# Kernel tuning notes

Hardware: AMD Instinct MI355X
Metric: run time of the kernel (lower is better)

## Reference

```python
import jax, jax.numpy as jnp
import numpy as np

N = 20000      # nodes
E = 320000     # edges (avg degree 16)
IN = 512       # input feature dim
HID = 64       # hidden_dim
NH = 8         # n_heads
NC = 20        # n_classes
NG = 64        # graphs in batch
EPS = 1e-5     # batchnorm eps


def setup_inputs() -> dict:
    key = jax.random.key(0)
    ks = jax.random.split(key, 32)
    rn = lambda k, shape, s=0.05: (jax.random.normal(k, shape, jnp.float32) * s)
    inp = {
        "x": rn(ks[0], (N, IN), 1.0),
        "src": jax.random.randint(ks[1], (E,), 0, N),
        "dst": jax.random.randint(ks[2], (E,), 0, N),
        "graph_ids": jnp.sort(jax.random.randint(ks[3], (N,), 0, NG)),
        "n_graphs": NG,
        # encoder
        "W_enc": rn(ks[4], (IN, HID)), "b_enc": jnp.zeros((HID,), jnp.float32),
        # GAT layer 0
        "fc_W0": rn(ks[5], (HID, NH * HID)),
        "attn_l0": rn(ks[6], (NH, HID)), "attn_r0": rn(ks[7], (NH, HID)),
        "res_W0": rn(ks[8], (HID, NH * HID)),
        "bias0": jnp.zeros((NH * HID,), jnp.float32),
        "dp_W0": rn(ks[9], (NH * HID, HID)), "dp_b0": jnp.zeros((HID,), jnp.float32),
        # GAT layer 1
        "fc_W1": rn(ks[10], (HID, NH * HID)),
        "attn_l1": rn(ks[11], (NH, HID)), "attn_r1": rn(ks[12], (NH, HID)),
        "res_W1": rn(ks[13], (HID, NH * HID)),
        "bias1": jnp.zeros((NH * HID,), jnp.float32),
        "dp_W1": rn(ks[14], (NH * HID, HID)), "dp_b1": jnp.zeros((HID,), jnp.float32),
        # batchnorm affine
        "gamma": jnp.ones((2 * HID,), jnp.float32), "beta": jnp.zeros((2 * HID,), jnp.float32),
        # global attention pooling gate
        "gate_W": rn(ks[15], (2 * HID, 1)), "gate_b": jnp.zeros((1,), jnp.float32),
        # classifier
        "cls_W": rn(ks[16], (2 * HID, NC)), "cls_b": jnp.zeros((NC,), jnp.float32),
    }
    return inp


def gat_conv(h, fc_W, attn_l, attn_r, res_W, bias, src, dst, n_nodes):
    # DGL GATConv: fc -> per-head scalar scores -> edge softmax over incoming
    # edges -> weighted sum -> residual + bias -> leaky_relu activation.
    nh, d = attn_l.shape
    feat = (h @ fc_W).reshape(n_nodes, nh, d)              # [N,H,D]
    el = jnp.sum(feat * attn_l[None], axis=-1)             # [N,H]
    er = jnp.sum(feat * attn_r[None], axis=-1)             # [N,H]
    e = jax.nn.leaky_relu(el[src] + er[dst], 0.2)          # [E,H]
    m = jax.ops.segment_max(e, dst, num_segments=n_nodes)  # segment softmax
    ex = jnp.exp(e - m[dst])
    denom = jax.ops.segment_sum(ex, dst, num_segments=n_nodes)
    a = ex / denom[dst]                                    # [E,H]
    msg = feat[src] * a[:, :, None]                        # [E,H,D]  (dominant)
    rst = jax.ops.segment_sum(msg, dst, num_segments=n_nodes)  # [N,H,D]
    rst = rst + (h @ res_W).reshape(n_nodes, nh, d) + bias.reshape(nh, d)
    return jax.nn.leaky_relu(rst, 0.01)  # F.leaky_relu default slope


def reference(x, W_enc, b_enc,
              fc_W0, attn_l0, attn_r0, res_W0, bias0, dp_W0, dp_b0,
              fc_W1, attn_l1, attn_r1, res_W1, bias1, dp_W1, dp_b1,
              gamma, beta, gate_W, gate_b, cls_W, cls_b,
              src, dst, graph_ids, n_graphs):
    n_nodes = x.shape[0]
    he = x @ W_enc + b_enc                                  # encoder [N,HID]
    h = he
    h = gat_conv(h, fc_W0, attn_l0, attn_r0, res_W0, bias0, src, dst, n_nodes)
    h = h.reshape(n_nodes, -1) @ dp_W0 + dp_b0              # down_proj 0
    h = gat_conv(h, fc_W1, attn_l1, attn_r1, res_W1, bias1, src, dst, n_nodes)
    h = h.reshape(n_nodes, -1) @ dp_W1 + dp_b1              # down_proj 1
    hg = jnp.concatenate([h, he], axis=1)                   # [N,2*HID]
    # BatchNorm1d (training-mode batch stats, biased variance)
    mu = jnp.mean(hg, axis=0)
    var = jnp.var(hg, axis=0)
    hg = (hg - mu) * jax.lax.rsqrt(var + EPS) * gamma + beta
    # GlobalAttentionPooling: per-graph softmax over node gates
    gate = hg @ gate_W + gate_b                             # [N,1]
    gm = jax.ops.segment_max(gate, graph_ids, num_segments=n_graphs)
    ge = jnp.exp(gate - gm[graph_ids])
    gden = jax.ops.segment_sum(ge, graph_ids, num_segments=n_graphs)
    alpha = ge / gden[graph_ids]                            # [N,1]
    readout = jax.ops.segment_sum(alpha * hg, graph_ids, num_segments=n_graphs)
    return readout @ cls_W + cls_b                          # [NG,NC]
```

## Files before the change

### kernel.cpp

```cpp
#include <hip/hip_runtime.h>
#include <hip/hip_bf16.h>

#define MROWS   20000
#define N_EDGES 320000
#define DIN     512
#define HID     64
#define NH      8
#define ND      512
#define NCLS    20
#define NG      64
#define BN_EPS  1e-5f
#define PCH     16
#define BNB     256
#define TPB     128

typedef __hip_bfloat16 bf16;
typedef __attribute__((ext_vector_type(8))) short s16x8;
typedef __attribute__((ext_vector_type(4))) short s16x4;
typedef __attribute__((ext_vector_type(4))) float f32x4;

enum { TF32 = 0, TBF16 = 1, TMODE = 2 };

__device__ __forceinline__ int is_bf16_mode(const void* gamma) {
    return *(const unsigned*)gamma != 0x3F800000u;
}

__device__ __forceinline__ float ld_f32(const void* p, size_t i) { return ((const float*)p)[i]; }
__device__ __forceinline__ float ld_b16(const void* p, size_t i) { return __bfloat162float(((const bf16*)p)[i]); }

template<int T>
__device__ __forceinline__ float ldT(const void* p, size_t i, int bf) {
    if constexpr (T == TF32) return ld_f32(p, i);
    else if constexpr (T == TBF16) return ld_b16(p, i);
    else return bf ? ld_b16(p, i) : ld_f32(p, i);
}
template<int T>
__device__ __forceinline__ void stT(void* p, size_t i, int bf, float v) {
    if constexpr (T == TF32) ((float*)p)[i] = v;
    else if constexpr (T == TBF16) ((bf16*)p)[i] = __float2bfloat16(v);
    else { if (bf) ((bf16*)p)[i] = __float2bfloat16(v); else ((float*)p)[i] = v; }
}

__device__ __forceinline__ float bfbits2f(short s) {
    return __uint_as_float(((unsigned)(unsigned short)s) << 16);
}
__device__ __forceinline__ short f2bfbits(float v) {
    bf16 b = __float2bfloat16(v);
    return *reinterpret_cast<short*>(&b);
}

struct TP { const void* src[7]; bf16* dst[7]; int K[7]; };
__global__ void prep_kernel(TP tp, const void* __restrict__ gamma, int* __restrict__ zero0) {
    int b = blockIdx.x;
    int z = b * 256 + threadIdx.x;
    if (z < 2 * MROWS) zero0[z] = 0;
    const int bf = is_bf16_mode(gamma);
    int id = b / TPB;
    int i = (b - id * TPB) * 256 + threadIdx.x;
    int K = tp.K[id];
    int N = (DIN * HID) / K;
    int n = i / K, k = i - n * K;
    tp.dst[id][i] = __float2bfloat16(ldT<TMODE>(tp.src[id], (size_t)k * N + n, bf));
}

__global__ void hist_kernel(const int* __restrict__ keys, int* __restrict__ counts, int n) {
    int i = blockIdx.x * 256 + threadIdx.x;
    if (i < n) atomicAdd(&counts[keys[i]], 1);
}

__global__ __launch_bounds__(1024)
void scan_all_kernel(const int* __restrict__ counts, int* __restrict__ offs,
                     const int* __restrict__ gids, int* __restrict__ goffs) {
    if (threadIdx.x <= NG) {
        int g = threadIdx.x;
        int lo = 0, hi = MROWS;
        while (lo < hi) {
            int mid = (lo + hi) >> 1;
            if (gids[mid] < g) lo = mid + 1; else hi = mid;
        }
        goffs[g] = lo;
    }
    __shared__ int wsum[16];
    __shared__ int carry_s;
    int carry = 0;
    int lane = threadIdx.x & 63, wid = threadIdx.x >> 6;
    const int NCHUNK = (MROWS + 1023) / 1024;
    for (int ch = 0; ch < NCHUNK; ++ch) {
        int i = ch * 1024 + threadIdx.x;
        int v = (i < MROWS) ? counts[i] : 0;
        int s = v;
        #pragma unroll
        for (int o = 1; o < 64; o <<= 1) { int t = __shfl_up(s, o, 64); if (lane >= o) s += t; }
        if (lane == 63) wsum[wid] = s;
        __syncthreads();
        if (wid == 0 && lane < 16) {
            int t = wsum[lane];
            #pragma unroll
            for (int o = 1; o < 16; o <<= 1) { int u = __shfl_up(t, o, 64); if (lane >= o) t += u; }
            wsum[lane] = t;
        }
        __syncthreads();
        int wc = (wid > 0) ? wsum[wid - 1] : 0;
        int incl = s + wc + carry;
        if (i < MROWS) offs[i] = incl - v;
        if (threadIdx.x == 1023) carry_s = incl;
        __syncthreads();
        carry = carry_s;
    }
    if (threadIdx.x == 0) offs[MROWS] = carry;
}

__global__ void scatter_kernel(const int* __restrict__ src, const int* __restrict__ dst,
                               const int* __restrict__ offs, int* __restrict__ cursor,
                               int* __restrict__ src_sorted) {
    int e = blockIdx.x * 256 + threadIdx.x;
    if (e < N_EDGES) {
        int d = dst[e];
        int pos = offs[d] + atomicAdd(&cursor[d], 1);
        src_sorted[pos] = src[e];
    }
}

template<int K, int NB, int NTOT, bool XF32>
__global__ __launch_bounds__(256)
void gemm_mfma(const void* __restrict__ Araw, const bf16* __restrict__ BT,
               const void* __restrict__ bias, bf16* __restrict__ C,
               const void* __restrict__ gamma) {
    const int bf = is_bf16_mode(gamma);
    const int wid  = threadIdx.x >> 6;
    const int lane = threadIdx.x & 63;
    const int quad = lane >> 4;
    const int l16  = lane & 15;
    const int rb = blockIdx.x * 128 + wid * 32;
    const int cb = blockIdx.y * NB;
    constexpr int CT = NB / 16;
    constexpr int KC = K / 32;

    f32x4 acc[2][CT] = {};
    int r0 = rb + l16;       if (r0 >= MROWS) r0 = MROWS - 1;
    int r1 = rb + 16 + l16;  if (r1 >= MROWS) r1 = MROWS - 1;

    auto lda = [&](int row, int koff) -> s16x8 {
        if (XF32 && !bf) {
            const float* fp = (const float*)Araw + (size_t)row * K + koff;
            float4 u = *(const float4*)fp;
            float4 v = *(const float4*)(fp + 4);
            s16x8 r;
            r[0] = f2bfbits(u.x); r[1] = f2bfbits(u.y); r[2] = f2bfbits(u.z); r[3] = f2bfbits(u.w);
            r[4] = f2bfbits(v.x); r[5] = f2bfbits(v.y); r[6] = f2bfbits(v.z); r[7] = f2bfbits(v.w);
            return r;
        }
        return *(const s16x8*)((const bf16*)Araw + (size_t)row * K + koff);
    };
    const bf16* btp = BT + (size_t)(cb + l16) * K + quad * 8;

    for (int kc = 0; kc < KC; ++kc) {
        s16x8 af0 = lda(r0, quad * 8 + kc * 32);
        s16x8 af1 = lda(r1, quad * 8 + kc * 32);
        s16x8 bfr[CT];
        #pragma unroll
        for (int ct = 0; ct < CT; ++ct)
            bfr[ct] = *(const s16x8*)(btp + (size_t)ct * 16 * K + kc * 32);
        #pragma unroll
        for (int ct = 0; ct < CT; ++ct) {
            acc[0][ct] = __builtin_amdgcn_mfma_f32_16x16x32_bf16(bfr[ct], af0, acc[0][ct], 0, 0, 0);
            acc[1][ct] = __builtin_amdgcn_mfma_f32_16x16x32_bf16(bfr[ct], af1, acc[1][ct], 0, 0, 0);
        }
    }
    #pragma unroll
    for (int ct = 0; ct < CT; ++ct) {
        int c0 = cb + ct * 16 + quad * 4;
        float b0 = bias ? ldT<TMODE>(bias, c0 + 0, bf) : 0.f;
        float b1 = bias ? ldT<TMODE>(bias, c0 + 1, bf) : 0.f;
        float b2 = bias ? ldT<TMODE>(bias, c0 + 2, bf) : 0.f;
        float b3 = bias ? ldT<TMODE>(bias, c0 + 3, bf) : 0.f;
        #pragma unroll
        for (int rt = 0; rt < 2; ++rt) {
            int row = rb + rt * 16 + l16;
            if (row < MROWS) {
                s16x4 o;
                o[0] = f2bfbits(acc[rt][ct][0] + b0);
                o[1] = f2bfbits(acc[rt][ct][1] + b1);
                o[2] = f2bfbits(acc[rt][ct][2] + b2);
                o[3] = f2bfbits(acc[rt][ct][3] + b3);
                *(s16x4*)(C + (size_t)row * NTOT + c0) = o;
            }
        }
    }
}

__global__ __launch_bounds__(256)
void gemm_fcres(const bf16* __restrict__ A, const bf16* __restrict__ BT_fc,
                const bf16* __restrict__ BT_res, const void* __restrict__ bias,
                const void* __restrict__ attn_l, const void* __restrict__ attn_r,
                bf16* __restrict__ feat, bf16* __restrict__ rst,
                float* __restrict__ el, float* __restrict__ er,
                const void* __restrict__ gamma) {
    const int bf = is_bf16_mode(gamma);
    const bool isres = blockIdx.y >= 4;
    const int yy = blockIdx.y & 3;
    const bf16* BT = isres ? BT_res : BT_fc;
    bf16* C = isres ? rst : feat;
    const int wid  = threadIdx.x >> 6;
    const int lane = threadIdx.x & 63;
    const int quad = lane >> 4;
    const int l16  = lane & 15;
    const int rb = blockIdx.x * 128 + wid * 32;
    const int cb = yy * 128;
    constexpr int CT = 8;
    constexpr int K  = HID;
    constexpr int KC = K / 32;

    f32x4 acc[2][CT] = {};
    int r0 = rb + l16;       if (r0 >= MROWS) r0 = MROWS - 1;
    int r1 = rb + 16 + l16;  if (r1 >= MROWS) r1 = MROWS - 1;
    const bf16* a0p = A + (size_t)r0 * K + quad * 8;
    const bf16* a1p = A + (size_t)r1 * K + quad * 8;
    const bf16* btp = BT + (size_t)(cb + l16) * K + quad * 8;

    #pragma unroll
    for (int kc = 0; kc < KC; ++kc) {
        s16x8 af0 = *(const s16x8*)(a0p + kc * 32);
        s16x8 af1 = *(const s16x8*)(a1p + kc * 32);
        s16x8 bfr[CT];
        #pragma unroll
        for (int ct = 0; ct < CT; ++ct)
            bfr[ct] = *(const s16x8*)(btp + (size_t)ct * 16 * K + kc * 32);
        #pragma unroll
        for (int ct = 0; ct < CT; ++ct) {
            acc[0][ct] = __builtin_amdgcn_mfma_f32_16x16x32_bf16(bfr[ct], af0, acc[0][ct], 0, 0, 0);
            acc[1][ct] = __builtin_amdgcn_mfma_f32_16x16x32_bf16(bfr[ct], af1, acc[1][ct], 0, 0, 0);
        }
    }
    #pragma unroll
    for (int ct = 0; ct < CT; ++ct) {
        int c0 = cb + ct * 16 + quad * 4;
        float b0 = isres ? ldT<TMODE>(bias, c0 + 0, bf) : 0.f;
        float b1 = isres ? ldT<TMODE>(bias, c0 + 1, bf) : 0.f;
        float b2 = isres ? ldT<TMODE>(bias, c0 + 2, bf) : 0.f;
        float b3 = isres ? ldT<TMODE>(bias, c0 + 3, bf) : 0.f;
        #pragma unroll
        for (int rt = 0; rt < 2; ++rt) {
            int row = rb + rt * 16 + l16;
            if (row < MROWS) {
                s16x4 o;
                o[0] = f2bfbits(acc[rt][ct][0] + b0);
                o[1] = f2bfbits(acc[rt][ct][1] + b1);
                o[2] = f2bfbits(acc[rt][ct][2] + b2);
                o[3] = f2bfbits(acc[rt][ct][3] + b3);
                *(s16x4*)(C + (size_t)row * ND + c0) = o;
            }
        }
    }
    if (!isres) {
        #pragma unroll
        for (int rt = 0; rt < 2; ++rt) {
            float e0 = 0.f, f0 = 0.f, e1 = 0.f, f1 = 0.f;
            #pragma unroll
            for (int ct = 0; ct < 4; ++ct) {
                int c0 = cb + ct * 16 + quad * 4;
                int c1 = c0 + 64;
                #pragma unroll
                for (int rg = 0; rg < 4; ++rg) {
                    e0 += acc[rt][ct][rg]     * ldT<TMODE>(attn_l, c0 + rg, bf);
                    f0 += acc[rt][ct][rg]     * ldT<TMODE>(attn_r, c0 + rg, bf);
                    e1 += acc[rt][ct + 4][rg] * ldT<TMODE>(attn_l, c1 + rg, bf);
                    f1 += acc[rt][ct + 4][rg] * ldT<TMODE>(attn_r, c1 + rg, bf);
                }
            }
            e0 += __shfl_xor(e0, 16, 64); e0 += __shfl_xor(e0, 32, 64);
            f0 += __shfl_xor(f0, 16, 64); f0 += __shfl_xor(f0, 32, 64);
            e1 += __shfl_xor(e1, 16, 64); e1 += __shfl_xor(e1, 32, 64);
            f1 += __shfl_xor(f1, 16, 64); f1 += __shfl_xor(f1, 32, 64);
            int row = rb + rt * 16 + l16;
            if (row < MROWS) {
                if (quad == 0)      el[row * 8 + 2 * yy]     = e0;
                else if (quad == 1) el[row * 8 + 2 * yy + 1] = e1;
                else if (quad == 2) er[row * 8 + 2 * yy]     = f0;
                else                er[row * 8 + 2 * yy + 1] = f1;
            }
        }
    }
}

__global__ __launch_bounds__(256)
void agg_kernel(const bf16* __restrict__ feat, const float* __restrict__ el,
                const float* __restrict__ er, const int* __restrict__ offs,
                const int* __restrict__ srcs, bf16* __restrict__ rst) {
    int gid = blockIdx.x * 256 + threadIdx.x;
    int n = gid >> 6;
    int l = threadIdx.x & 63;
    if (n >= MROWS) return;
    int hh = l >> 3;
    int e0 = __builtin_amdgcn_readfirstlane(offs[n]);
    int e1 = __builtin_amdgcn_readfirstlane(offs[n + 1]);
    float er_h = er[n * 8 + hh];
    float acc[8] = {0.f, 0.f, 0.f, 0.f, 0.f, 0.f, 0.f, 0.f};
    float den = 0.f;
    for (int base = e0; base < e1; base += 64) {
        int cnt = min(64, e1 - base);
        int sv = (base + l < e1) ? srcs[base + l] : 0;
        for (int eb = 0; eb < cnt; eb += 8) {
            int en = cnt - eb;
            s16x8 ff[8];
            float elv[8];
            int lastv = cnt - 1;
            #pragma unroll
            for (int p = 0; p < 8; ++p) {
                int idx = eb + p; if (idx > lastv) idx = lastv;
                int s = __shfl(sv, idx, 64);
                ff[p] = *(const s16x8*)(feat + (size_t)s * ND + l * 8);
                elv[p] = el[s * 8 + hh];
            }
            float ww[8];
            #pragma unroll
            for (int p = 0; p < 8; ++p) {
                float sc = elv[p] + er_h;
                sc = sc > 0.f ? sc : 0.2f * sc;
                ww[p] = __expf(fminf(sc, 30.f));
            }
            if (en < 8) {
                #pragma unroll
                for (int p = 1; p < 8; ++p)
                    if (p >= en) ww[p] = 0.f;
            }
            #pragma unroll
            for (int p = 0; p < 8; ++p) {
                den += ww[p];
                #pragma unroll
                for (int j = 0; j < 8; ++j)
                    acc[j] += bfbits2f(ff[p][j]) * ww[p];
            }
        }
    }
    float inv = (den > 0.f) ? 1.f / den : 0.f;
    s16x8* rp = (s16x8*)(rst + (size_t)n * ND + l * 8);
    s16x8 rr = *rp;
    s16x8 ro;
    #pragma unroll
    for (int j = 0; j < 8; ++j) {
        float r = bfbits2f(rr[j]) + acc[j] * inv;
        r = r > 0.f ? r : 0.01f * r;
        ro[j] = f2bfbits(r);
    }
    *rp = ro;
}

__global__ void bn_part_kernel(const bf16* __restrict__ h2, const bf16* __restrict__ he,
                               float* __restrict__ psum, float* __restrict__ psq) {
    int t = threadIdx.x;
    int b = blockIdx.x;
    int beg = (int)((long)MROWS * b / BNB);
    int end = (int)((long)MROWS * (b + 1) / BNB);
    const bf16* srcb = (t < 64) ? h2 : he;
    int col = t & 63;
    float s = 0.f, s2 = 0.f;
    for (int r = beg; r < end; ++r) {
        float v = __bfloat162float(srcb[(size_t)r * 64 + col]);
        s += v;
        s2 += v * v;
    }
    psum[b * 128 + t] = s;
    psq[b * 128 + t] = s2;
}

__global__ void bn_reduce_kernel(const float* __restrict__ psum, const float* __restrict__ psq,
                                 const void* __restrict__ gamma, const void* __restrict__ beta,
                                 float* __restrict__ scale, float* __restrict__ shift) {
    const int bf = is_bf16_mode(gamma);
    int t = threadIdx.x;
    float s = 0.f, s2 = 0.f;
    for (int b = 0; b < BNB; ++b) { s += psum[b * 128 + t]; s2 += psq[b * 128 + t]; }
    float mu = s * (1.f / MROWS);
    float var = s2 * (1.f / MROWS) - mu * mu;
    float inv = rsqrtf(fmaxf(var, 0.f) + BN_EPS);
    float a = ldT<TMODE>(gamma, t, bf) * inv;
    scale[t] = a;
    shift[t] = ldT<TMODE>(beta, t, bf) - mu * a;
}

__global__ __launch_bounds__(128)
void poolgate_kernel(const bf16* __restrict__ h2, const bf16* __restrict__ he,
                     const float* __restrict__ scale, const float* __restrict__ shift,
                     const void* __restrict__ gate_W, const void* __restrict__ gate_b,
                     const int* __restrict__ goffs,
                     float* __restrict__ pacc, float* __restrict__ pden,
                     const void* __restrict__ gamma) {
    const int bf = is_bf16_mode(gamma);
    int g = blockIdx.x;
    int c = blockIdx.y;
    int t = threadIdx.x;
    int r0 = goffs[g], r1 = goffs[g + 1];
    int len = r1 - r0;
    int beg = r0 + (int)((long)len * c / PCH);
    int end = r0 + (int)((long)len * (c + 1) / PCH);
    const bf16* srcb = (t < 64) ? h2 : he;
    int col = t & 63;
    float sc = scale[t], sh = shift[t];
    float gw = ldT<TMODE>(gate_W, t, bf);
    float gb = ldT<TMODE>(gate_b, 0, bf);
    __shared__ float ws[2];
    float acc = 0.f, den = 0.f;
    for (int r = beg; r < end; ++r) {
        float v = __bfloat162float(srcb[(size_t)r * 64 + col]) * sc + sh;
        float p = v * gw;
        #pragma unroll
        for (int o = 32; o > 0; o >>= 1) p += __shfl_xor(p, o, 64);
        if ((t & 63) == 0) ws[t >> 6] = p;
        __syncthreads();
        float wg = __expf(fminf(fmaxf(ws[0] + ws[1] + gb, -60.f), 30.f));
        den += wg;
        acc += wg * v;
        __syncthreads();
    }
    pacc[((size_t)g * PCH + c) * 128 + t] = acc;
    if (t == 0) pden[g * PCH + c] = den;
}

__global__ __launch_bounds__(128)
void poolcls_kernel(const float* __restrict__ pacc, const float* __restrict__ pden,
                    const void* __restrict__ W, const void* __restrict__ b,
                    void* __restrict__ out, const void* __restrict__ gamma) {
    const int bf = is_bf16_mode(gamma);
    int g = blockIdx.x;
    int t = threadIdx.x;
    float acc = 0.f, den = 0.f;
    #pragma unroll
    for (int c = 0; c < PCH; ++c) {
        acc += pacc[((size_t)g * PCH + c) * 128 + t];
        den += pden[g * PCH + c];
    }
    __shared__ float rs[128];
    rs[t] = (den > 0.f) ? acc / den : 0.f;
    __syncthreads();
    if (t < NCLS) {
        float o = ldT<TMODE>(b, t, bf);
        #pragma unroll 8
        for (int k = 0; k < 128; ++k)
            o += rs[k] * ldT<TMODE>(W, (size_t)k * NCLS + t, bf);
        stT<TMODE>(out, g * NCLS + t, bf, o);
    }
}

extern "C" void kernel_launch(void* const* d_in, const int* in_sizes, int n_in,
                              void* d_out, int out_size, void* d_ws, size_t ws_size,
                              hipStream_t stream) {
    const void* x       = d_in[0];
    const int*  src     = (const int*)d_in[1];
    const int*  dst     = (const int*)d_in[2];
    const int*  gids    = (const int*)d_in[3];
    const void* W_enc   = d_in[5];
    const void* b_enc   = d_in[6];
    const void* fc_W0   = d_in[7];
    const void* attn_l0 = d_in[8];
    const void* attn_r0 = d_in[9];
    const void* res_W0  = d_in[10];
    const void* bias0   = d_in[11];
    const void* dp_W0   = d_in[12];
    const void* dp_b0   = d_in[13];
    const void* fc_W1   = d_in[14];
    const void* attn_l1 = d_in[15];
    const void* attn_r1 = d_in[16];
    const void* res_W1  = d_in[17];
    const void* bias1   = d_in[18];
    const void* dp_W1   = d_in[19];
    const void* dp_b1   = d_in[20];
    const void* gamma   = d_in[21];
    const void* beta    = d_in[22];
    const void* gate_W  = d_in[23];
    const void* gate_b  = d_in[24];
    const void* cls_W   = d_in[25];
    const void* cls_b   = d_in[26];

    char* wsc = (char*)d_ws;
    size_t off = 0;
    auto alloc = [&](size_t bytes) -> void* {
        void* p = wsc + off;
        off = (off + bytes + 255) & ~(size_t)255;
        return p;
    };
    bf16*  he        = (bf16*) alloc((size_t)MROWS * HID * 2);
    bf16*  h         = (bf16*) alloc((size_t)MROWS * HID * 2);
    bf16*  h2        = (bf16*) alloc((size_t)MROWS * HID * 2);
    bf16*  feat      = (bf16*) alloc((size_t)MROWS * ND * 2);
    bf16*  rst       = (bf16*) alloc((size_t)MROWS * ND * 2);
    bf16*  bt_enc    = (bf16*) alloc((size_t)DIN * HID * 2);
    bf16*  bt_fc0    = (bf16*) alloc((size_t)HID * ND * 2);
    bf16*  bt_res0   = (bf16*) alloc((size_t)HID * ND * 2);
    bf16*  bt_dp0    = (bf16*) alloc((size_t)ND * HID * 2);
    bf16*  bt_fc1    = (bf16*) alloc((size_t)HID * ND * 2);
    bf16*  bt_res1   = (bf16*) alloc((size_t)HID * ND * 2);
    bf16*  bt_dp1    = (bf16*) alloc((size_t)ND * HID * 2);
    float* el        = (float*)alloc((size_t)MROWS * 8 * 4);
    float* er        = (float*)alloc((size_t)MROWS * 8 * 4);
    int*   src_sorted= (int*)  alloc((size_t)N_EDGES * 4);
    int*   offs      = (int*)  alloc((size_t)(MROWS + 1) * 4);
    int*   goffs     = (int*)  alloc((size_t)(NG + 1) * 4);
    float* psum      = (float*)alloc((size_t)BNB * 128 * 4);
    float* psq       = (float*)alloc((size_t)BNB * 128 * 4);
    float* pacc      = (float*)alloc((size_t)NG * PCH * 128 * 4);
    float* pden      = (float*)alloc((size_t)NG * PCH * 4);
    float* bnscale   = (float*)alloc(128 * 4);
    float* bnshift   = (float*)alloc(128 * 4);
    char*  zbase     = (char*) alloc((size_t)MROWS * 4 * 2);
    int* counts  = (int*)zbase;
    int* cursor  = counts + MROWS;

    TP tp;
    tp.src[0] = W_enc;  tp.K[0] = DIN;
    tp.src[1] = fc_W0;  tp.K[1] = HID;
    tp.src[2] = res_W0; tp.K[2] = HID;
    tp.src[3] = dp_W0;  tp.K[3] = ND;
    tp.src[4] = fc_W1;  tp.K[4] = HID;
    tp.src[5] = res_W1; tp.K[5] = HID;
    tp.src[6] = dp_W1;  tp.K[6] = ND;
    tp.dst[0] = bt_enc; tp.dst[1] = bt_fc0; tp.dst[2] = bt_res0; tp.dst[3] = bt_dp0;
    tp.dst[4] = bt_fc1; tp.dst[5] = bt_res1; tp.dst[6] = bt_dp1;
    prep_kernel<<<7 * TPB, 256, 0, stream>>>(tp, gamma, (int*)zbase);

    hist_kernel<<<(N_EDGES + 255) / 256, 256, 0, stream>>>(dst, counts, N_EDGES);
    scan_all_kernel<<<1, 1024, 0, stream>>>(counts, offs, gids, goffs);
    scatter_kernel<<<(N_EDGES + 255) / 256, 256, 0, stream>>>(src, dst, offs, cursor, src_sorted);

    const int GX = (MROWS + 127) / 128;

    gemm_mfma<DIN, 64, 64, true><<<dim3(GX, 1), 256, 0, stream>>>(x, bt_enc, b_enc, he, gamma);

    gemm_fcres<<<dim3(GX, 8), 256, 0, stream>>>(he, bt_fc0, bt_res0, bias0, attn_l0, attn_r0,
                                                feat, rst, el, er, gamma);
    agg_kernel<<<(MROWS * 64) / 256, 256, 0, stream>>>(feat, el, er, offs, src_sorted, rst);
    gemm_mfma<ND, 64, 64, false><<<dim3(GX, 1), 256, 0, stream>>>(rst, bt_dp0, dp_b0, h, gamma);

    gemm_fcres<<<dim3(GX, 8), 256, 0, stream>>>(h, bt_fc1, bt_res1, bias1, attn_l1, attn_r1,
                                                feat, rst, el, er, gamma);
    agg_kernel<<<(MROWS * 64) / 256, 256, 0, stream>>>(feat, el, er, offs, src_sorted, rst);
    gemm_mfma<ND, 64, 64, false><<<dim3(GX, 1), 256, 0, stream>>>(rst, bt_dp1, dp_b1, h2, gamma);

    bn_part_kernel<<<BNB, 128, 0, stream>>>(h2, he, psum, psq);
    bn_reduce_kernel<<<1, 128, 0, stream>>>(psum, psq, gamma, beta, bnscale, bnshift);
    poolgate_kernel<<<dim3(NG, PCH), 128, 0, stream>>>(h2, he, bnscale, bnshift, gate_W, gate_b,
                                                       goffs, pacc, pden, gamma);
    poolcls_kernel<<<NG, 128, 0, stream>>>(pacc, pden, cls_W, cls_b, d_out, gamma);
}
```

Baseline: 470.2 us.

## Split GAT aggregation per head across blocks with 8-lane node groups

The edge-softmax aggregation kernel now gives each block a single head and a chunk of 160 nodes. Each 8-lane group handles one node's 64 head features and walks its incoming edges four at a time. Previously a whole wave processed one node across all heads and shared source indices through shuffles. The new mapping is meant to give more independent node streams per wave and keep each block's gathers within one head's feature slice, which should help L2 locality. In exchange, every lane group reloads source indices and el values itself, and each 16-byte gather covers only one head's slice of a source row.

```diff
diff --git a/kernel.cpp b/kernel.cpp
--- a/kernel.cpp
+++ b/kernel.cpp
@@ -13,6 +13,8 @@
 #define PCH     16
 #define BNB     256
 #define TPB     128
+#define AGG_NBLK  125
+#define AGG_CHUNK 160
 
 typedef __hip_bfloat16 bf16;
 typedef __attribute__((ext_vector_type(8))) short s16x8;
@@ -287,63 +289,62 @@
 void agg_kernel(const bf16* __restrict__ feat, const float* __restrict__ el,
                 const float* __restrict__ er, const int* __restrict__ offs,
                 const int* __restrict__ srcs, bf16* __restrict__ rst) {
-    int gid = blockIdx.x * 256 + threadIdx.x;
-    int n = gid >> 6;
-    int l = threadIdx.x & 63;
-    if (n >= MROWS) return;
-    int hh = l >> 3;
-    int e0 = __builtin_amdgcn_readfirstlane(offs[n]);
-    int e1 = __builtin_amdgcn_readfirstlane(offs[n + 1]);
-    float er_h = er[n * 8 + hh];
-    float acc[8] = {0.f, 0.f, 0.f, 0.f, 0.f, 0.f, 0.f, 0.f};
-    float den = 0.f;
-    for (int base = e0; base < e1; base += 64) {
-        int cnt = min(64, e1 - base);
-        int sv = (base + l < e1) ? srcs[base + l] : 0;
-        for (int eb = 0; eb < cnt; eb += 8) {
-            int en = cnt - eb;
-            s16x8 ff[8];
-            float elv[8];
-            int lastv = cnt - 1;
+    const int b = blockIdx.x;
+    const int hx = b & 7;
+    const int chunk = b >> 3;
+    const int g = threadIdx.x >> 3;
+    const int l8 = threadIdx.x & 7;
+    const int base = hx * 64 + l8 * 8;
+
+    for (int n = chunk * AGG_CHUNK + g; n < (chunk + 1) * AGG_CHUNK; n += 32) {
+        int e0 = offs[n], e1 = offs[n + 1];
+        float er_h = er[n * 8 + hx];
+        float acc[8] = {0.f, 0.f, 0.f, 0.f, 0.f, 0.f, 0.f, 0.f};
+        float den = 0.f;
+        for (int eb = e0; eb < e1; eb += 4) {
+            int last = e1 - 1;
+            int i1 = eb + 1 > last ? last : eb + 1;
+            int i2 = eb + 2 > last ? last : eb + 2;
+            int i3 = eb + 3 > last ? last : eb + 3;
+            int s0 = srcs[eb], s1 = srcs[i1], s2 = srcs[i2], s3 = srcs[i3];
+            float l0 = el[s0 * 8 + hx], l1 = el[s1 * 8 + hx];
+            float l2 = el[s2 * 8 + hx], l3 = el[s3 * 8 + hx];
+            s16x8 f0 = *(const s16x8*)(feat + (size_t)s0 * ND + base);
+            s16x8 f1 = *(const s16x8*)(feat + (size_t)s1 * ND + base);
+            s16x8 f2 = *(const s16x8*)(feat + (size_t)s2 * ND + base);
+            s16x8 f3 = *(const s16x8*)(feat + (size_t)s3 * ND + base);
+            float sc0 = l0 + er_h; sc0 = sc0 > 0.f ? sc0 : 0.2f * sc0;
+            float sc1 = l1 + er_h; sc1 = sc1 > 0.f ? sc1 : 0.2f * sc1;
+            float sc2 = l2 + er_h; sc2 = sc2 > 0.f ? sc2 : 0.2f * sc2;
+            float sc3 = l3 + er_h; sc3 = sc3 > 0.f ? sc3 : 0.2f * sc3;
+            float w0 = __expf(fminf(sc0, 30.f));
+            float w1 = __expf(fminf(sc1, 30.f));
+            float w2 = __expf(fminf(sc2, 30.f));
+            float w3 = __expf(fminf(sc3, 30.f));
+            int rem = e1 - eb;
+            if (rem < 4) {
+                if (rem < 2) w1 = 0.f;
+                if (rem < 3) w2 = 0.f;
+                w3 = 0.f;
+            }
+            den += w0 + w1 + w2 + w3;
             #pragma unroll
-            for (int p = 0; p < 8; ++p) {
-                int idx = eb + p; if (idx > lastv) idx = lastv;
-                int s = __shfl(sv, idx, 64);
-                ff[p] = *(const s16x8*)(feat + (size_t)s * ND + l * 8);
-                elv[p] = el[s * 8 + hh];
-            }
-            float ww[8];
-            #pragma unroll
-            for (int p = 0; p < 8; ++p) {
-                float sc = elv[p] + er_h;
-                sc = sc > 0.f ? sc : 0.2f * sc;
-                ww[p] = __expf(fminf(sc, 30.f));
-            }
-            if (en < 8) {
-                #pragma unroll
-                for (int p = 1; p < 8; ++p)
-                    if (p >= en) ww[p] = 0.f;
-            }
-            #pragma unroll
-            for (int p = 0; p < 8; ++p) {
-                den += ww[p];
-                #pragma unroll
-                for (int j = 0; j < 8; ++j)
-                    acc[j] += bfbits2f(ff[p][j]) * ww[p];
-            }
-        }
-    }
-    float inv = (den > 0.f) ? 1.f / den : 0.f;
-    s16x8* rp = (s16x8*)(rst + (size_t)n * ND + l * 8);
-    s16x8 rr = *rp;
-    s16x8 ro;
-    #pragma unroll
-    for (int j = 0; j < 8; ++j) {
-        float r = bfbits2f(rr[j]) + acc[j] * inv;
-        r = r > 0.f ? r : 0.01f * r;
-        ro[j] = f2bfbits(r);
-    }
-    *rp = ro;
+            for (int j = 0; j < 8; ++j)
+                acc[j] += bfbits2f(f0[j]) * w0 + bfbits2f(f1[j]) * w1
+                        + bfbits2f(f2[j]) * w2 + bfbits2f(f3[j]) * w3;
+        }
+        float inv = (den > 0.f) ? 1.f / den : 0.f;
+        s16x8* rp = (s16x8*)(rst + (size_t)n * ND + base);
+        s16x8 rr = *rp;
+        s16x8 ro;
+        #pragma unroll
+        for (int j = 0; j < 8; ++j) {
+            float r = bfbits2f(rr[j]) + acc[j] * inv;
+            r = r > 0.f ? r : 0.01f * r;
+            ro[j] = f2bfbits(r);
+        }
+        *rp = ro;
+    }
 }
 
 __global__ void bn_part_kernel(const bf16* __restrict__ h2, const bf16* __restrict__ he,
@@ -528,12 +529,12 @@
 
     gemm_fcres<<<dim3(GX, 8), 256, 0, stream>>>(he, bt_fc0, bt_res0, bias0, attn_l0, attn_r0,
                                                 feat, rst, el, er, gamma);
-    agg_kernel<<<(MROWS * 64) / 256, 256, 0, stream>>>(feat, el, er, offs, src_sorted, rst);
+    agg_kernel<<<AGG_NBLK * 8, 256, 0, stream>>>(feat, el, er, offs, src_sorted, rst);
     gemm_mfma<ND, 64, 64, false><<<dim3(GX, 1), 256, 0, stream>>>(rst, bt_dp0, dp_b0, h, gamma);
 
     gemm_fcres<<<dim3(GX, 8), 256, 0, stream>>>(h, bt_fc1, bt_res1, bias1, attn_l1, attn_r1,
                                                 feat, rst, el, er, gamma);
-    agg_kernel<<<(MROWS * 64) / 256, 256, 0, stream>>>(feat, el, er, offs, src_sorted, rst);
+    agg_kernel<<<AGG_NBLK * 8, 256, 0, stream>>>(feat, el, er, offs, src_sorted, rst);
     gemm_mfma<ND, 64, 64, false><<<dim3(GX, 1), 256, 0, stream>>>(rst, bt_dp1, dp_b1, h2, gamma);
 
     bn_part_kernel<<<BNB, 128, 0, stream>>>(h2, he, psum, psq);
```

Measured after the change: 468.3 us. No clear change (-0.4%).
